# Performance work log

Measured on AMD Instinct MI355X. Metric: run time of the kernel, lower is better.

## Reference

```python
import jax, jax.numpy as jnp
import numpy as np

N = 8192       # num nodes
F_IN = 256     # num_features
NHID = 128     # nhid
E = 524288     # num edges (avg degree 64)
K = 32         # num_edge_preseve


def setup_inputs() -> dict:
    key = jax.random.key(0)
    ks = jax.random.split(key, 5)
    x = jax.random.normal(ks[0], (N, F_IN), jnp.float32)
    edge_index = jax.random.randint(ks[1], (2, E), 0, N, jnp.int32)
    W1 = jax.random.normal(ks[2], (F_IN, NHID), jnp.float32) / np.sqrt(F_IN)
    b1 = jnp.zeros((NHID,), jnp.float32)
    We = jax.random.normal(ks[3], (2 * NHID, 1), jnp.float32) / np.sqrt(2 * NHID)
    be = jnp.zeros((1,), jnp.float32)
    return {"x": x, "edge_index": edge_index, "W1": W1, "b1": b1, "We": We, "be": be}


def _segment_sparsemax(z, seg, num_segments):
    """Sparsemax applied independently within each segment (row) of an edge list."""
    E_ = z.shape[0]
    # group edges by segment, descending score within segment
    order = jnp.lexsort((-z, seg))
    zs = z[order]
    ss = seg[order]
    counts = jnp.zeros((num_segments,), jnp.int32).at[seg].add(1)
    starts = jnp.cumsum(counts) - counts                 # first sorted index of each segment
    pos = jnp.arange(E_, dtype=jnp.int32) - starts[ss]   # 0-based rank within segment
    cs = jnp.cumsum(zs)
    prefix = cs - zs                                     # cumsum excluding self
    seg_cs = cs - prefix[starts][ss]                     # within-segment inclusive cumsum
    j1 = (pos + 1).astype(zs.dtype)
    cond = 1.0 + j1 * zs > seg_cs                        # sparsemax support condition
    kmax = jax.ops.segment_max(jnp.where(cond, pos + 1, 0), ss, num_segments=num_segments)
    kmax = jnp.maximum(kmax, 1)                          # nonempty segments always have k>=1
    idx = jnp.clip(starts + kmax - 1, 0, E_ - 1)
    seg_cs_at_k = cs[idx] - prefix[jnp.clip(starts, 0, E_ - 1)]
    tau = (seg_cs_at_k - 1.0) / kmax.astype(zs.dtype)
    out_sorted = jnp.maximum(zs - tau[ss], 0.0)
    return jnp.zeros_like(z).at[order].set(out_sorted)


def reference(x, edge_index, W1, b1, We, be):
    h = jax.nn.relu(x @ W1 + b1)                 # [N, NHID]
    row, col = edge_index[0], edge_index[1]
    # edge score: Linear on concat([h[row], h[col]]) == split matmul (avoids [E, 2*NHID] concat)
    e = h[row] @ We[:NHID, 0] + h[col] @ We[NHID:, 0] + be[0]   # [E]
    scores = _segment_sparsemax(e, row, N)       # row-segmented sparsemax
    adj = jnp.zeros((N, N), h.dtype).at[row, col].set(scores)
    topv = jax.lax.top_k(adj, K)[0]              # [N, K], sorted descending
    thresh = topv[:, -1:]                        # per-row k-th largest value
    new_adj = jnp.where(adj >= thresh, adj, jnp.zeros((), adj.dtype))
    # original returns dense_to_sparse(new_adj) (data-dependent shape);
    # we return the equivalent masked dense adjacency.
    return h, new_adj
```

## Files before the change

kernel.cpp:

```cpp
#include <hip/hip_runtime.h>

#define N_    8192
#define FIN_  256
#define NHID_ 128
#define E_    524288
#define KTOP  32
#define CAP   160

__global__ __launch_bounds__(256) void k_gemm_ab(const float* __restrict__ x,
                                                 const float* __restrict__ W1,
                                                 const float* __restrict__ b1,
                                                 const float* __restrict__ We,
                                                 float* __restrict__ h,
                                                 float* __restrict__ a,
                                                 float* __restrict__ b,
                                                 int* __restrict__ cnt) {
    __shared__ float xs[8][FIN_];
    int t = threadIdx.x;
    int row0 = blockIdx.x * 8;
    const float4* xg = (const float4*)(x + (size_t)row0 * FIN_);
    float4* xs4 = (float4*)&xs[0][0];
    xs4[t]       = xg[t];
    xs4[t + 256] = xg[t + 256];
    if (t < 8) cnt[row0 + t] = 0;
    __syncthreads();
    int row = t >> 5;
    int jg  = t & 31;
    const float* wp = W1 + jg * 4;
    float4 acc = *(const float4*)(b1 + jg * 4);
    const float* xr = xs[row];
#pragma unroll 8
    for (int k = 0; k < FIN_; ++k) {
        float4 w = *(const float4*)(wp + (size_t)k * NHID_);
        float xv = xr[k];
        acc.x = fmaf(xv, w.x, acc.x);
        acc.y = fmaf(xv, w.y, acc.y);
        acc.z = fmaf(xv, w.z, acc.z);
        acc.w = fmaf(xv, w.w, acc.w);
    }
    acc.x = fmaxf(acc.x, 0.f);
    acc.y = fmaxf(acc.y, 0.f);
    acc.z = fmaxf(acc.z, 0.f);
    acc.w = fmaxf(acc.w, 0.f);
    *(float4*)(h + (size_t)(row0 + row) * NHID_ + jg * 4) = acc;

    float4 we1 = *(const float4*)(We + jg * 4);
    float4 we2 = *(const float4*)(We + NHID_ + jg * 4);
    float p = acc.x * we1.x + acc.y * we1.y + acc.z * we1.z + acc.w * we1.w;
    float q = acc.x * we2.x + acc.y * we2.y + acc.z * we2.z + acc.w * we2.w;
#pragma unroll
    for (int o = 16; o > 0; o >>= 1) {
        p += __shfl_down(p, o, 32);
        q += __shfl_down(q, o, 32);
    }
    if (jg == 0) { a[row0 + row] = p; b[row0 + row] = q; }
}

__global__ __launch_bounds__(256) void k_scatter(const int* __restrict__ ei,
                                                 int* __restrict__ cnt,
                                                 int* __restrict__ ecol) {
    int e = blockIdx.x * 256 + threadIdx.x;
    int r = ei[e];
    int c = ei[E_ + e];
    int pos = atomicAdd(&cnt[r], 1);
    if (pos < CAP) ecol[r * CAP + pos] = c;
}

__global__ __launch_bounds__(256) void k_rows(const int* __restrict__ cnt,
                                              const int* __restrict__ ecol,
                                              const float* __restrict__ a,
                                              const float* __restrict__ b,
                                              const float* __restrict__ be,
                                              float* __restrict__ adj) {
    __shared__ float zs[CAP];
    __shared__ int   cols[CAP];
    __shared__ float srt[CAP];
    __shared__ unsigned char dupf[CAP];
    __shared__ float s_tau, s_thresh;

    int r = blockIdx.x;
    int t = threadIdx.x;
    int m = cnt[r];
    if (m > CAP) m = CAP;

    float* row = adj + (size_t)r * N_;
    float4* row4 = (float4*)row;
    float4 z4 = make_float4(0.f, 0.f, 0.f, 0.f);
#pragma unroll
    for (int i = 0; i < 8; ++i) row4[t + 256 * i] = z4;

    float ab = a[r] + be[0];
    for (int i = t; i < m; i += 256) {
        int c = ecol[r * CAP + i];
        cols[i] = c;
        zs[i] = ab + b[c];
    }
    __syncthreads();
    if (m == 0) return;

    for (int i = t; i < m; i += 256) {
        float zi = zs[i];
        int ci = cols[i];
        int rank = 0;
        for (int jj = 0; jj < m; ++jj) {
            float zj = zs[jj];
            rank += (zj > zi) || (zj == zi && jj < i);
        }
        bool dup = false;
        for (int jj = 0; jj < i; ++jj)
            if (cols[jj] == ci) { dup = true; break; }
        srt[rank] = zi;
        dupf[i] = dup ? 1 : 0;
    }
    __syncthreads();

    if (t == 0) {
        float c = 0.f;
        int kmax = 1;
        float csk = srt[0];
        for (int jj = 0; jj < m; ++jj) {
            c += srt[jj];
            if (1.0f + (float)(jj + 1) * srt[jj] > c) { kmax = jj + 1; csk = c; }
        }
        s_tau = (csk - 1.0f) / (float)kmax;
        s_thresh = 0.f;
    }
    __syncthreads();
    float tau = s_tau;

    for (int i = t; i < m; i += 256) {
        if (dupf[i]) continue;
        float zi = zs[i];
        int rank = 0;
        for (int jj = 0; jj < m; ++jj) {
            if (dupf[jj] || jj == i) continue;
            float zj = zs[jj];
            rank += (zj > zi) || (zj == zi && jj < i);
        }
        if (rank == KTOP - 1) {
            float s = zi - tau;
            s_thresh = s > 0.f ? s : 0.f;
        }
    }
    __syncthreads();
    float thresh = s_thresh;

    for (int i = t; i < m; i += 256) {
        float s = zs[i] - tau;
        if (s > 0.f && s >= thresh) row[cols[i]] = s;
    }
}

extern "C" void kernel_launch(void* const* d_in, const int* in_sizes, int n_in,
                              void* d_out, int out_size, void* d_ws, size_t ws_size,
                              hipStream_t stream) {
    const float* x  = (const float*)d_in[0];
    const int*   ei = (const int*)d_in[1];
    const float* W1 = (const float*)d_in[2];
    const float* b1 = (const float*)d_in[3];
    const float* We = (const float*)d_in[4];
    const float* be = (const float*)d_in[5];

    float* h_out   = (float*)d_out;
    float* adj_out = h_out + (size_t)N_ * NHID_;

    float* a    = (float*)d_ws;
    float* b    = a + N_;
    int*   cnt  = (int*)(b + N_);
    int*   ecol = cnt + N_;

    k_gemm_ab<<<N_ / 8, 256, 0, stream>>>(x, W1, b1, We, h_out, a, b, cnt);
    k_scatter<<<E_ / 256, 256, 0, stream>>>(ei, cnt, ecol);
    k_rows   <<<N_, 256, 0, stream>>>(cnt, ecol, a, b, be, adj_out);
}
```

Measured before the change: 386.4 us.

## Process one row per wavefront in k_rows instead of one row per block

Each 256-thread block now handles four adjacent rows, one per 64-lane wavefront, with shared arrays split per wave and block-wide barriers replaced by wave shuffles for tau and the threshold. With average degree 64, most of the block's 256 threads previously sat idle on per-row loops. This should raise lane utilization and cut the number of blocks. The cost is that each wave zeroes a full 32KB row by itself and loops over edges only 64 at a time.

```diff
diff --git a/kernel.cpp b/kernel.cpp
--- a/kernel.cpp
+++ b/kernel.cpp
@@ -72,14 +72,14 @@
                                               const float* __restrict__ b,
                                               const float* __restrict__ be,
                                               float* __restrict__ adj) {
-    __shared__ float zs[CAP];
-    __shared__ int   cols[CAP];
-    __shared__ float srt[CAP];
-    __shared__ unsigned char dupf[CAP];
-    __shared__ float s_tau, s_thresh;
+    __shared__ float zs[4][CAP];
+    __shared__ int   cols[4][CAP];
+    __shared__ float srt[4][CAP];
+    __shared__ int   dupf[4][CAP];
 
-    int r = blockIdx.x;
     int t = threadIdx.x;
+    int wave = t >> 6, lane = t & 63;
+    int r = blockIdx.x * 4 + wave;
     int m = cnt[r];
     if (m > CAP) m = CAP;
 
@@ -87,67 +87,69 @@
     float4* row4 = (float4*)row;
     float4 z4 = make_float4(0.f, 0.f, 0.f, 0.f);
 #pragma unroll
-    for (int i = 0; i < 8; ++i) row4[t + 256 * i] = z4;
+    for (int i = 0; i < 32; ++i) row4[lane + 64 * i] = z4;
 
-    float ab = a[r] + be[0];
-    for (int i = t; i < m; i += 256) {
-        int c = ecol[r * CAP + i];
-        cols[i] = c;
-        zs[i] = ab + b[c];
+    float tau = 0.f, thresh = 0.f;
+    if (m > 0) {
+        float ab = a[r] + be[0];
+        for (int i = lane; i < m; i += 64) {
+            int c = ecol[r * CAP + i];
+            cols[wave][i] = c;
+            zs[wave][i] = ab + b[c];
+        }
+        for (int i = lane; i < m; i += 64) {
+            float zi = zs[wave][i];
+            int ci = cols[wave][i];
+            int rank = 0;
+            for (int jj = 0; jj < m; ++jj) {
+                float zj = zs[wave][jj];
+                rank += (zj > zi) || (zj == zi && jj < i);
+            }
+            int dup = 0;
+            for (int jj = 0; jj < i; ++jj)
+                if (cols[wave][jj] == ci) { dup = 1; break; }
+            srt[wave][rank] = zi;
+            dupf[wave][i] = dup;
+        }
+        if (lane == 0) {
+            float c = 0.f;
+            int kmax = 1;
+            float csk = srt[wave][0];
+            for (int jj = 0; jj < m; ++jj) {
+                c += srt[wave][jj];
+                if (1.0f + (float)(jj + 1) * srt[wave][jj] > c) { kmax = jj + 1; csk = c; }
+            }
+            tau = (csk - 1.0f) / (float)kmax;
+        }
+        tau = __shfl(tau, 0);
+
+        float cand = 0.f;
+        for (int i = lane; i < m; i += 64) {
+            if (dupf[wave][i]) continue;
+            float zi = zs[wave][i];
+            int rank = 0;
+            for (int jj = 0; jj < m; ++jj) {
+                if (dupf[wave][jj] || jj == i) continue;
+                float zj = zs[wave][jj];
+                rank += (zj > zi) || (zj == zi && jj < i);
+            }
+            if (rank == KTOP - 1) {
+                float s = zi - tau;
+                cand = s > 0.f ? s : 0.f;
+            }
+        }
+#pragma unroll
+        for (int o = 32; o > 0; o >>= 1) cand = fmaxf(cand, __shfl_down(cand, o));
+        thresh = __shfl(cand, 0);
     }
-    __syncthreads();
-    if (m == 0) return;
 
-    for (int i = t; i < m; i += 256) {
-        float zi = zs[i];
-        int ci = cols[i];
-        int rank = 0;
-        for (int jj = 0; jj < m; ++jj) {
-            float zj = zs[jj];
-            rank += (zj > zi) || (zj == zi && jj < i);
-        }
-        bool dup = false;
-        for (int jj = 0; jj < i; ++jj)
-            if (cols[jj] == ci) { dup = true; break; }
-        srt[rank] = zi;
-        dupf[i] = dup ? 1 : 0;
-    }
     __syncthreads();
 
-    if (t == 0) {
-        float c = 0.f;
-        int kmax = 1;
-        float csk = srt[0];
-        for (int jj = 0; jj < m; ++jj) {
-            c += srt[jj];
-            if (1.0f + (float)(jj + 1) * srt[jj] > c) { kmax = jj + 1; csk = c; }
+    if (m > 0) {
+        for (int i = lane; i < m; i += 64) {
+            float s = zs[wave][i] - tau;
+            if (s > 0.f && s >= thresh) row[cols[wave][i]] = s;
         }
-        s_tau = (csk - 1.0f) / (float)kmax;
-        s_thresh = 0.f;
-    }
-    __syncthreads();
-    float tau = s_tau;
-
-    for (int i = t; i < m; i += 256) {
-        if (dupf[i]) continue;
-        float zi = zs[i];
-        int rank = 0;
-        for (int jj = 0; jj < m; ++jj) {
-            if (dupf[jj] || jj == i) continue;
-            float zj = zs[jj];
-            rank += (zj > zi) || (zj == zi && jj < i);
-        }
-        if (rank == KTOP - 1) {
-            float s = zi - tau;
-            s_thresh = s > 0.f ? s : 0.f;
-        }
-    }
-    __syncthreads();
-    float thresh = s_thresh;
-
-    for (int i = t; i < m; i += 256) {
-        float s = zs[i] - tau;
-        if (s > 0.f && s >= thresh) row[cols[i]] = s;
     }
 }
 
@@ -171,5 +173,5 @@
 
     k_gemm_ab<<<N_ / 8, 256, 0, stream>>>(x, W1, b1, We, h_out, a, b, cnt);
     k_scatter<<<E_ / 256, 256, 0, stream>>>(ei, cnt, ecol);
-    k_rows   <<<N_, 256, 0, stream>>>(cnt, ecol, a, b, be, adj_out);
+    k_rows   <<<N_ / 4, 256, 0, stream>>>(cnt, ecol, a, b, be, adj_out);
 }
```

Result: no change. 392.5 us (+1.6%).

## Fuse edge scatter into GEMM kernel with two rows per thread

Applied to the files above, without the earlier changes.

Merges the edge-bucketing scatter into the projection GEMM kernel. Each of 512 blocks scatters 1024 edges using int4 loads and then computes 16 rows of h, with each thread accumulating two rows so every W1 load is reused twice. The count reset moves to a hipMemsetAsync because the scatter now runs in the same kernel that used to zero cnt. This removes one kernel launch and halves W1 traffic, but adds a memset call and gives the GEMM fewer blocks.

```diff
diff --git a/kernel.cpp b/kernel.cpp
--- a/kernel.cpp
+++ b/kernel.cpp
@@ -7,63 +7,82 @@
 #define KTOP  32
 #define CAP   160
 
-__global__ __launch_bounds__(256) void k_gemm_ab(const float* __restrict__ x,
-                                                 const float* __restrict__ W1,
-                                                 const float* __restrict__ b1,
-                                                 const float* __restrict__ We,
-                                                 float* __restrict__ h,
-                                                 float* __restrict__ a,
-                                                 float* __restrict__ b,
-                                                 int* __restrict__ cnt) {
-    __shared__ float xs[8][FIN_];
+__global__ __launch_bounds__(256) void k_fused(const float* __restrict__ x,
+                                               const int* __restrict__ ei,
+                                               const float* __restrict__ W1,
+                                               const float* __restrict__ b1,
+                                               const float* __restrict__ We,
+                                               float* __restrict__ h,
+                                               float* __restrict__ a,
+                                               float* __restrict__ b,
+                                               int* __restrict__ cnt,
+                                               int* __restrict__ ecol) {
+    __shared__ float xs[16][FIN_];
     int t = threadIdx.x;
-    int row0 = blockIdx.x * 8;
+    int blk = blockIdx.x;
+
+    {
+        int4 r4 = ((const int4*)ei)[blk * 256 + t];
+        int4 c4 = ((const int4*)(ei + E_))[blk * 256 + t];
+        int p;
+        p = atomicAdd(&cnt[r4.x], 1); if (p < CAP) ecol[r4.x * CAP + p] = c4.x;
+        p = atomicAdd(&cnt[r4.y], 1); if (p < CAP) ecol[r4.y * CAP + p] = c4.y;
+        p = atomicAdd(&cnt[r4.z], 1); if (p < CAP) ecol[r4.z * CAP + p] = c4.z;
+        p = atomicAdd(&cnt[r4.w], 1); if (p < CAP) ecol[r4.w * CAP + p] = c4.w;
+    }
+
+    int row0 = blk * 16;
     const float4* xg = (const float4*)(x + (size_t)row0 * FIN_);
     float4* xs4 = (float4*)&xs[0][0];
-    xs4[t]       = xg[t];
-    xs4[t + 256] = xg[t + 256];
-    if (t < 8) cnt[row0 + t] = 0;
+#pragma unroll
+    for (int i = 0; i < 4; ++i) xs4[t + 256 * i] = xg[t + 256 * i];
     __syncthreads();
-    int row = t >> 5;
-    int jg  = t & 31;
+
+    int rg = t >> 5;
+    int jg = t & 31;
+    int r0 = 2 * rg, r1 = 2 * rg + 1;
     const float* wp = W1 + jg * 4;
-    float4 acc = *(const float4*)(b1 + jg * 4);
-    const float* xr = xs[row];
+    float4 bb = *(const float4*)(b1 + jg * 4);
+    float4 acc0 = bb, acc1 = bb;
+    const float* xr0 = xs[r0];
+    const float* xr1 = xs[r1];
 #pragma unroll 8
     for (int k = 0; k < FIN_; ++k) {
         float4 w = *(const float4*)(wp + (size_t)k * NHID_);
-        float xv = xr[k];
-        acc.x = fmaf(xv, w.x, acc.x);
-        acc.y = fmaf(xv, w.y, acc.y);
-        acc.z = fmaf(xv, w.z, acc.z);
-        acc.w = fmaf(xv, w.w, acc.w);
+        float x0 = xr0[k], x1 = xr1[k];
+        acc0.x = fmaf(x0, w.x, acc0.x);
+        acc0.y = fmaf(x0, w.y, acc0.y);
+        acc0.z = fmaf(x0, w.z, acc0.z);
+        acc0.w = fmaf(x0, w.w, acc0.w);
+        acc1.x = fmaf(x1, w.x, acc1.x);
+        acc1.y = fmaf(x1, w.y, acc1.y);
+        acc1.z = fmaf(x1, w.z, acc1.z);
+        acc1.w = fmaf(x1, w.w, acc1.w);
     }
-    acc.x = fmaxf(acc.x, 0.f);
-    acc.y = fmaxf(acc.y, 0.f);
-    acc.z = fmaxf(acc.z, 0.f);
-    acc.w = fmaxf(acc.w, 0.f);
-    *(float4*)(h + (size_t)(row0 + row) * NHID_ + jg * 4) = acc;
+    acc0.x = fmaxf(acc0.x, 0.f); acc0.y = fmaxf(acc0.y, 0.f);
+    acc0.z = fmaxf(acc0.z, 0.f); acc0.w = fmaxf(acc0.w, 0.f);
+    acc1.x = fmaxf(acc1.x, 0.f); acc1.y = fmaxf(acc1.y, 0.f);
+    acc1.z = fmaxf(acc1.z, 0.f); acc1.w = fmaxf(acc1.w, 0.f);
+    *(float4*)(h + (size_t)(row0 + r0) * NHID_ + jg * 4) = acc0;
+    *(float4*)(h + (size_t)(row0 + r1) * NHID_ + jg * 4) = acc1;
 
     float4 we1 = *(const float4*)(We + jg * 4);
     float4 we2 = *(const float4*)(We + NHID_ + jg * 4);
-    float p = acc.x * we1.x + acc.y * we1.y + acc.z * we1.z + acc.w * we1.w;
-    float q = acc.x * we2.x + acc.y * we2.y + acc.z * we2.z + acc.w * we2.w;
+    float p0 = acc0.x * we1.x + acc0.y * we1.y + acc0.z * we1.z + acc0.w * we1.w;
+    float q0 = acc0.x * we2.x + acc0.y * we2.y + acc0.z * we2.z + acc0.w * we2.w;
+    float p1 = acc1.x * we1.x + acc1.y * we1.y + acc1.z * we1.z + acc1.w * we1.w;
+    float q1 = acc1.x * we2.x + acc1.y * we2.y + acc1.z * we2.z + acc1.w * we2.w;
 #pragma unroll
     for (int o = 16; o > 0; o >>= 1) {
-        p += __shfl_down(p, o, 32);
-        q += __shfl_down(q, o, 32);
+        p0 += __shfl_down(p0, o, 32);
+        q0 += __shfl_down(q0, o, 32);
+        p1 += __shfl_down(p1, o, 32);
+        q1 += __shfl_down(q1, o, 32);
     }
-    if (jg == 0) { a[row0 + row] = p; b[row0 + row] = q; }
-}
-
-__global__ __launch_bounds__(256) void k_scatter(const int* __restrict__ ei,
-                                                 int* __restrict__ cnt,
-                                                 int* __restrict__ ecol) {
-    int e = blockIdx.x * 256 + threadIdx.x;
-    int r = ei[e];
-    int c = ei[E_ + e];
-    int pos = atomicAdd(&cnt[r], 1);
-    if (pos < CAP) ecol[r * CAP + pos] = c;
+    if (jg == 0) {
+        a[row0 + r0] = p0; b[row0 + r0] = q0;
+        a[row0 + r1] = p1; b[row0 + r1] = q1;
+    }
 }
 
 __global__ __launch_bounds__(256) void k_rows(const int* __restrict__ cnt,
@@ -169,7 +188,7 @@
     int*   cnt  = (int*)(b + N_);
     int*   ecol = cnt + N_;
 
-    k_gemm_ab<<<N_ / 8, 256, 0, stream>>>(x, W1, b1, We, h_out, a, b, cnt);
-    k_scatter<<<E_ / 256, 256, 0, stream>>>(ei, cnt, ecol);
-    k_rows   <<<N_, 256, 0, stream>>>(cnt, ecol, a, b, be, adj_out);
+    hipMemsetAsync(cnt, 0, N_ * sizeof(int), stream);
+    k_fused<<<512, 256, 0, stream>>>(x, ei, W1, b1, We, h_out, a, b, cnt, ecol);
+    k_rows <<<N_, 256, 0, stream>>>(cnt, ecol, a, b, be, adj_out);
 }
```

Measured after the change: 375.5 us. 2.8% less time.
